# Kernel tuning notes

Hardware: AMD Instinct MI355X
Metric: run time of the kernel (lower is better)

The kernel has to match this reference:

```python
import jax, jax.numpy as jnp
import numpy as np

N = 20000      # nodes
E = 400000     # directed edges
F_IN = 256     # node features
H, C = 16, 32  # heads, per-head channels (out_channels + beta_on, beta_on=0)
OUT = 32       # out_channels
HID = 128      # 4 * out_channels


def setup_inputs() -> dict:
    key = jax.random.key(0)
    ks = jax.random.split(key, 14)
    s = 0.05
    return {
        "x": jax.random.normal(ks[0], (N, F_IN), jnp.float32),
        "edge_index": jax.random.randint(ks[1], (2, E), 0, N, jnp.int32),
        "W1": jax.random.normal(ks[2], (F_IN, H * C), jnp.float32) * s,
        "att_src1": jax.random.normal(ks[3], (H, C), jnp.float32) * s,
        "att_dst1": jax.random.normal(ks[4], (H, C), jnp.float32) * s,
        "b1": jax.random.normal(ks[5], (C,), jnp.float32) * s,
        "W2": jax.random.normal(ks[6], (F_IN, H * C), jnp.float32) * s,
        "att_src2": jax.random.normal(ks[7], (H, C), jnp.float32) * s,
        "att_dst2": jax.random.normal(ks[8], (H, C), jnp.float32) * s,
        "b2": jax.random.normal(ks[9], (C,), jnp.float32) * s,
        "lin1_w": jax.random.normal(ks[10], (F_IN, HID), jnp.float32) * s,
        "lin1_b": jax.random.normal(ks[11], (HID,), jnp.float32) * s,
        "lin2_w": jax.random.normal(ks[12], (HID, OUT), jnp.float32) * s,
        "lin2_b": jax.random.normal(ks[13], (OUT,), jnp.float32) * s,
    }


def gat_conv(x, W, att_src, att_dst, bias, src, dst):
    """PyG GATConv: heads=H, concat=False (mean over heads), no self loops.
    src = message source node per edge, dst = aggregation (central) node."""
    h = (x @ W).reshape(-1, H, C)                 # [N, H, C]
    a_s = jnp.sum(h * att_src, axis=-1)           # [N, H]
    a_d = jnp.sum(h * att_dst, axis=-1)           # [N, H]
    alpha = jax.nn.leaky_relu(a_s[src] + a_d[dst], 0.2)  # [E, H]
    # numerically-stable segment softmax over edges grouped by dst
    m = jax.lax.stop_gradient(jax.ops.segment_max(alpha, dst, num_segments=N))
    m = jnp.where(jnp.isfinite(m), m, 0.0)        # empty segments -> -inf
    ex = jnp.exp(alpha - m[dst])                  # [E, H]
    den = jax.ops.segment_sum(ex, dst, num_segments=N)   # [N, H]
    coef = ex / (den[dst] + 1e-16)                # [E, H]
    msg = h[src] * coef[:, :, None]               # [E, H, C]
    out = jax.ops.segment_sum(msg, dst, num_segments=N)  # [N, H, C]
    return out.mean(axis=1) + bias                # concat=False -> head mean


def reference(x, edge_index, W1, att_src1, att_dst1, b1, W2, att_src2, att_dst2,
              b2, lin1_w, lin1_b, lin2_w, lin2_b):
    src = edge_index[0]
    dst = edge_index[1]
    # conv1: flow='source_to_target' -> aggregate at edge_index[1]
    x_in = jax.nn.elu(gat_conv(x, W1, att_src1, att_dst1, b1, src, dst))
    # conv2: flow='target_to_source' -> aggregate at edge_index[0]
    x_out = jax.nn.elu(gat_conv(x, W2, att_src2, att_dst2, b2, dst, src))
    x1 = jax.nn.elu(x @ lin1_w + lin1_b)
    x_self = jax.nn.elu(x1 @ lin2_w + lin2_b)
    return (x_in, x_out, x_self)
```

## Files before the change

kernel.cpp:

```cpp
#include <hip/hip_runtime.h>
#include <math.h>

#define NN 20000
#define EE 400000
#define FIN 256
#define HH 16
#define CC 32
#define HC 512
#define H8W 1024
#define HIDN 128
#define OUTC 32
#define WT 1024
#define GEMM_B 1256

typedef unsigned short u16;
typedef unsigned char u8;
typedef __attribute__((ext_vector_type(8))) short short8v;
typedef __attribute__((ext_vector_type(4))) float f32x4;
typedef __attribute__((ext_vector_type(2))) float f32x2;

__device__ inline u16 f2bf(float f) {
  unsigned u = __builtin_bit_cast(unsigned, f);
  unsigned r = (u + 0x7fffu + ((u >> 16) & 1u)) >> 16;
  return (u16)r;
}

__device__ __forceinline__ void gload16(const u16* g, u16* l) {
  __builtin_amdgcn_global_load_lds(
      (const __attribute__((address_space(1))) unsigned int*)g,
      (__attribute__((address_space(3))) unsigned int*)l, 16, 0, 0);
}

__device__ __forceinline__ void fp8x8_fma2(uint2 hv, float w, f32x2* acc) {
  f32x2 w2; w2.x = w; w2.y = w;
  f32x2 p0 = __builtin_amdgcn_cvt_pk_f32_fp8(hv.x, false);
  f32x2 p1 = __builtin_amdgcn_cvt_pk_f32_fp8(hv.x, true);
  f32x2 p2 = __builtin_amdgcn_cvt_pk_f32_fp8(hv.y, false);
  f32x2 p3 = __builtin_amdgcn_cvt_pk_f32_fp8(hv.y, true);
  acc[0] += p0 * w2;
  acc[1] += p1 * w2;
  acc[2] += p2 * w2;
  acc[3] += p3 * w2;
}

__global__ void k_prep_hist(const float* __restrict__ x, u16* __restrict__ xb,
                            const float* __restrict__ W1, const float* __restrict__ W2,
                            u16* __restrict__ wtc,
                            const float* __restrict__ L1, u16* __restrict__ lt1,
                            const float* __restrict__ L2, u16* __restrict__ lt2,
                            const int* __restrict__ ei, int* __restrict__ cur) {
  int b = blockIdx.x, t = threadIdx.x;
  if (b < 2500) {
    int i = b * 256 + t;
    float4 v0 = ((const float4*)x)[i * 2];
    float4 v1 = ((const float4*)x)[i * 2 + 1];
    short8v o;
    o[0] = (short)f2bf(v0.x); o[1] = (short)f2bf(v0.y);
    o[2] = (short)f2bf(v0.z); o[3] = (short)f2bf(v0.w);
    o[4] = (short)f2bf(v1.x); o[5] = (short)f2bf(v1.y);
    o[6] = (short)f2bf(v1.z); o[7] = (short)f2bf(v1.w);
    *(short8v*)(xb + (size_t)i * 8) = o;
  } else if (b < 3524) {
    int i = (b - 2500) * 256 + t;
    int n = i >> 8, k = i & 255;
    wtc[i] = f2bf(n < 512 ? W1[k * HC + n] : W2[k * HC + (n - 512)]);
  } else if (b < 3652) {
    int i = (b - 3524) * 256 + t;
    int n = i >> 8, k = i & 255;
    lt1[i] = f2bf(L1[k * HIDN + n]);
  } else if (b < 3668) {
    int i = (b - 3652) * 256 + t;
    int n = i >> 7, k = i & 127;
    lt2[i] = f2bf(L2[k * OUTC + n]);
  } else {
    int e = (b - 3668) * 256 + t;
    if (e < EE) {
      atomicAdd(&cur[ei[EE + e]], 1);
      atomicAdd(&cur[NN + ei[e]], 1);
    }
  }
}

__device__ void scan_one(int* cur, int* off, int* part) {
  const int t = threadIdx.x;
  const int CHK = 20;
  int base = t * CHK;
  int loc[CHK];
  int s = 0;
#pragma unroll
  for (int i = 0; i < CHK; ++i) {
    int idx = base + i;
    int v = (idx < NN) ? cur[idx] : 0;
    loc[i] = s;
    s += v;
  }
  part[t] = s;
  __syncthreads();
  for (int d = 1; d < 1024; d <<= 1) {
    int v2 = (t >= d) ? part[t - d] : 0;
    __syncthreads();
    part[t] += v2;
    __syncthreads();
  }
  int cbase = part[t] - s;
#pragma unroll
  for (int i = 0; i < CHK; ++i) {
    int idx = base + i;
    if (idx < NN) {
      int o = cbase + loc[i];
      off[idx] = o;
      cur[idx] = o;
    }
  }
  if (t == 1023) off[NN] = part[1023];
}

__global__ __launch_bounds__(1024) void k_scan(int* cur, int* off1, int* off2) {
  __shared__ int part[1024];
  if (blockIdx.x == 0) scan_one(cur, off1, part);
  else                 scan_one(cur + NN, off2, part);
}

__global__ __launch_bounds__(256) void k_gemm_big(const u16* __restrict__ A,
                                                  const u16* __restrict__ Bt,
                                                  const float* __restrict__ as1,
                                                  const float* __restrict__ ad1,
                                                  const float* __restrict__ as2,
                                                  const float* __restrict__ ad2,
                                                  u8* __restrict__ h8,
                                                  float* __restrict__ a_sA,
                                                  float* __restrict__ a_dA,
                                                  const int* __restrict__ ei,
                                                  int* __restrict__ cur,
                                                  int* __restrict__ adj1,
                                                  int* __restrict__ adj2) {
  __shared__ u16 As[128 * 64];
  __shared__ u16 Bs[128 * 64];
  const int hw = blockIdx.x;
  const int logical = (hw & 7) * 157 + (hw >> 3);
  const int bm = (logical >> 3) * 128, bn = logical & 7;
  const int t = threadIdx.x;
  const int lane = t & 63, wave = t >> 6;
  const int wr = (wave >> 1) * 64, wc = (wave & 1) * 64;
  const int l15 = lane & 15, l4 = lane >> 4;
  const int rloc = lane >> 3;
  const int kc_src = (lane & 7) ^ rloc;
  const int K = FIN;

  for (int e = hw * 256 + t; e < EE; e += GEMM_B * 256) {
    int s1 = ei[e], d1 = ei[EE + e];
    int p1 = atomicAdd(&cur[d1], 1);
    adj1[p1] = s1;
    int p2 = atomicAdd(&cur[NN + s1], 1);
    adj2[p2] = d1;
  }

  f32x4 acc[4][4] = {};
  for (int k0 = 0; k0 < K; k0 += 64) {
    __syncthreads();
#pragma unroll
    for (int q = 0; q < 4; ++q) {
      const int rblk = q * 4 + wave;
      const int r = rblk * 8 + rloc;
      gload16(A + (size_t)(bm + r) * K + k0 + kc_src * 8, As + rblk * 512);
      gload16(Bt + (size_t)(bn * 128 + r) * K + k0 + kc_src * 8, Bs + rblk * 512);
    }
    __syncthreads();
#pragma unroll
    for (int kh = 0; kh < 2; ++kh) {
      const int kc = kh * 4 + l4;
      short8v af[4], bfr[4];
#pragma unroll
      for (int i = 0; i < 4; ++i) {
        int row = wr + i * 16 + l15;
        af[i] = *(const short8v*)(As + row * 64 + (kc ^ (row & 7)) * 8);
      }
#pragma unroll
      for (int j = 0; j < 4; ++j) {
        int row = wc + j * 16 + l15;
        bfr[j] = *(const short8v*)(Bs + row * 64 + (kc ^ (row & 7)) * 8);
      }
#pragma unroll
      for (int i = 0; i < 4; ++i)
#pragma unroll
        for (int j = 0; j < 4; ++j)
          acc[i][j] = __builtin_amdgcn_mfma_f32_16x16x32_bf16(af[i], bfr[j], acc[i][j], 0, 0, 0);
    }
  }

  const int conv = bn >> 2;
#pragma unroll
  for (int i = 0; i < 4; ++i)
#pragma unroll
    for (int j = 0; j < 4; ++j)
#pragma unroll
      for (int r = 0; r < 4; ++r) {
        int row = bm + wr + i * 16 + l4 * 4 + r;
        if (row >= NN) continue;
        int colb = bn * 128 + wc + j * 16 + l15;
        float v = acc[i][j][r];
        unsigned e8 = __builtin_amdgcn_cvt_pk_fp8_f32(v, v, 0, false);
        h8[(size_t)row * H8W + colb] = (u8)e8;
      }

  float asv[4], adv[4];
#pragma unroll
  for (int j = 0; j < 4; ++j) {
    int lc = (bn & 3) * 128 + wc + j * 16 + l15;
    int hh = lc >> 5, c = lc & 31;
    asv[j] = (conv ? as2 : as1)[hh * CC + c];
    adv[j] = (conv ? ad2 : ad1)[hh * CC + c];
  }
  const int hA = (bn & 3) * 4 + (wc >> 5);
  float* aS = a_sA + (size_t)conv * NN * HH;
  float* aD = a_dA + (size_t)conv * NN * HH;
#pragma unroll
  for (int i = 0; i < 4; ++i)
#pragma unroll
    for (int r = 0; r < 4; ++r) {
      float sAs = acc[i][0][r] * asv[0] + acc[i][1][r] * asv[1];
      float sAd = acc[i][0][r] * adv[0] + acc[i][1][r] * adv[1];
      float sBs = acc[i][2][r] * asv[2] + acc[i][3][r] * asv[3];
      float sBd = acc[i][2][r] * adv[2] + acc[i][3][r] * adv[3];
#pragma unroll
      for (int m = 1; m < 16; m <<= 1) {
        sAs += __shfl_xor(sAs, m);
        sAd += __shfl_xor(sAd, m);
        sBs += __shfl_xor(sBs, m);
        sBd += __shfl_xor(sBd, m);
      }
      int row = bm + wr + i * 16 + l4 * 4 + r;
      if (l15 == 0 && row < NN) {
        *(float2*)(aS + (size_t)row * HH + hA) = make_float2(sAs, sBs);
        *(float2*)(aD + (size_t)row * HH + hA) = make_float2(sAd, sBd);
      }
    }
}

__global__ __launch_bounds__(256) void k_self(const u16* __restrict__ A,
                                              const u16* __restrict__ lt1,
                                              const u16* __restrict__ lt2,
                                              const float* __restrict__ lin1_b,
                                              const float* __restrict__ lin2_b,
                                              float* __restrict__ outp) {
  __shared__ u16 smem[128 * 136];
  u16* As = smem;
  u16* Bs = smem + 128 * 64;
  const int t = threadIdx.x;
  const int lane = t & 63, wave = t >> 6;
  const int wr = (wave >> 1) * 64, wc = (wave & 1) * 64;
  const int bm = blockIdx.x * 128;
  const int l15 = lane & 15, l4 = lane >> 4;
  const int rloc = lane >> 3;
  const int kc_src = (lane & 7) ^ rloc;
  const int K = FIN;

  f32x4 acc[4][4] = {};
  for (int k0 = 0; k0 < K; k0 += 64) {
    __syncthreads();
#pragma unroll
    for (int q = 0; q < 4; ++q) {
      const int rblk = q * 4 + wave;
      const int r = rblk * 8 + rloc;
      gload16(A + (size_t)(bm + r) * K + k0 + kc_src * 8, As + rblk * 512);
      gload16(lt1 + (size_t)r * K + k0 + kc_src * 8, Bs + rblk * 512);
    }
    __syncthreads();
#pragma unroll
    for (int kh = 0; kh < 2; ++kh) {
      const int kc = kh * 4 + l4;
      short8v af[4], bfr[4];
#pragma unroll
      for (int i = 0; i < 4; ++i) {
        int row = wr + i * 16 + l15;
        af[i] = *(const short8v*)(As + row * 64 + (kc ^ (row & 7)) * 8);
      }
#pragma unroll
      for (int j = 0; j < 4; ++j) {
        int row = wc + j * 16 + l15;
        bfr[j] = *(const short8v*)(Bs + row * 64 + (kc ^ (row & 7)) * 8);
      }
#pragma unroll
      for (int i = 0; i < 4; ++i)
#pragma unroll
        for (int j = 0; j < 4; ++j)
          acc[i][j] = __builtin_amdgcn_mfma_f32_16x16x32_bf16(af[i], bfr[j], acc[i][j], 0, 0, 0);
    }
  }
  __syncthreads();
#pragma unroll
  for (int i = 0; i < 4; ++i)
#pragma unroll
    for (int j = 0; j < 4; ++j)
#pragma unroll
      for (int r = 0; r < 4; ++r) {
        int row = wr + i * 16 + l4 * 4 + r;
        int col = wc + j * 16 + l15;
        float v = acc[i][j][r] + lin1_b[col];
        v = v > 0.f ? v : (expf(v) - 1.f);
        smem[row * 136 + col] = f2bf(v);
      }
  __syncthreads();
  f32x4 acc2[2][2] = {};
#pragma unroll
  for (int kk = 0; kk < 4; ++kk) {
    short8v af[2], bfr[2];
#pragma unroll
    for (int i = 0; i < 2; ++i)
      af[i] = *(const short8v*)(smem + (wave * 32 + i * 16 + l15) * 136 + kk * 32 + l4 * 8);
#pragma unroll
    for (int j = 0; j < 2; ++j)
      bfr[j] = *(const short8v*)(lt2 + (size_t)(j * 16 + l15) * 128 + kk * 32 + l4 * 8);
#pragma unroll
    for (int i = 0; i < 2; ++i)
#pragma unroll
      for (int j = 0; j < 2; ++j)
        acc2[i][j] = __builtin_amdgcn_mfma_f32_16x16x32_bf16(af[i], bfr[j], acc2[i][j], 0, 0, 0);
  }
#pragma unroll
  for (int i = 0; i < 2; ++i)
#pragma unroll
    for (int j = 0; j < 2; ++j)
#pragma unroll
      for (int r = 0; r < 4; ++r) {
        int row = bm + wave * 32 + i * 16 + l4 * 4 + r;
        int col = j * 16 + l15;
        if (row < NN) {
          float v = acc2[i][j][r] + lin2_b[col];
          v = v > 0.f ? v : (expf(v) - 1.f);
          outp[(size_t)row * OUTC + col] = v;
        }
      }
}

__global__ __launch_bounds__(256) void k_edge(const int* __restrict__ adj1,
                                              const int* __restrict__ off1,
                                              const int* __restrict__ adj2,
                                              const int* __restrict__ off2,
                                              const float* __restrict__ a_sA,
                                              const float* __restrict__ a_dA,
                                              const u8* __restrict__ h8,
                                              const float* __restrict__ b1,
                                              const float* __restrict__ b2,
                                              float* __restrict__ out) {
  const int wv = threadIdx.x >> 6, lane = threadIdx.x & 63;
  const int gid = blockIdx.x * 4 + wv;
  const int conv = gid >= NN;
  const int node = gid - conv * NN;
  const int* __restrict__ adj = conv ? adj2 : adj1;
  const int* __restrict__ off = conv ? off2 : off1;
  const float* __restrict__ a_s = a_sA + (size_t)conv * NN * HH;
  const float* __restrict__ a_d = a_dA + (size_t)conv * NN * HH;
  const float* __restrict__ bias = conv ? b2 : b1;
  float* __restrict__ outp = out + (size_t)conv * NN * OUTC;
  const int e0 = off[node], e1 = off[node + 1];

  const int ea = lane >> 4, hh = lane & 15;
  const int h = lane >> 2, cg = lane & 3;
  const u8* hb = h8 + conv * HC + h * CC + cg * 8;
  const float adh = a_d[node * HH + hh];
  f32x2 acc0[4] = {}, acc1[4] = {};
  float den = 0.f;
  int p = e0;
  for (; p + 4 <= e1; p += 4) {
    int se = adj[p + ea];
    float al = a_s[se * HH + hh] + adh;
    al = al > 0.f ? al : 0.2f * al;
    float wgt = __expf(al);
    den += wgt;
    float w0 = __shfl(wgt, h);
    float w1 = __shfl(wgt, 16 + h);
    float w2 = __shfl(wgt, 32 + h);
    float w3 = __shfl(wgt, 48 + h);
    int s0 = adj[p], s1 = adj[p + 1], s2 = adj[p + 2], s3 = adj[p + 3];
    uint2 h0 = *(const uint2*)(hb + (size_t)s0 * H8W);
    uint2 h1 = *(const uint2*)(hb + (size_t)s1 * H8W);
    uint2 h2v = *(const uint2*)(hb + (size_t)s2 * H8W);
    uint2 h3 = *(const uint2*)(hb + (size_t)s3 * H8W);
    fp8x8_fma2(h0, w0, acc0);
    fp8x8_fma2(h1, w1, acc1);
    fp8x8_fma2(h2v, w2, acc0);
    fp8x8_fma2(h3, w3, acc1);
  }
  if (p < e1) {
    int pe = p + ea;
    float wgt = 0.f;
    if (pe < e1) {
      int se = adj[pe];
      float al = a_s[se * HH + hh] + adh;
      al = al > 0.f ? al : 0.2f * al;
      wgt = __expf(al);
    }
    den += wgt;
    float w0 = __shfl(wgt, h);
    float w1 = __shfl(wgt, 16 + h);
    float w2 = __shfl(wgt, 32 + h);
    {
      int s0 = adj[p];
      uint2 h0 = *(const uint2*)(hb + (size_t)s0 * H8W);
      fp8x8_fma2(h0, w0, acc0);
    }
    if (p + 1 < e1) {
      int s1 = adj[p + 1];
      uint2 h1 = *(const uint2*)(hb + (size_t)s1 * H8W);
      fp8x8_fma2(h1, w1, acc1);
    }
    if (p + 2 < e1) {
      int s2 = adj[p + 2];
      uint2 h2v = *(const uint2*)(hb + (size_t)s2 * H8W);
      fp8x8_fma2(h2v, w2, acc0);
    }
  }
  den += __shfl_xor(den, 16);
  den += __shfl_xor(den, 32);
  float inv = (1.f / 16.f) / (den + 1e-16f);
  const float ivh = __shfl(inv, h);
  float accf[8];
#pragma unroll
  for (int i = 0; i < 4; ++i) {
    f32x2 s2v = acc0[i] + acc1[i];
    accf[2 * i] = s2v.x * ivh;
    accf[2 * i + 1] = s2v.y * ivh;
  }
#pragma unroll
  for (int mk = 4; mk <= 32; mk <<= 1)
#pragma unroll
    for (int i = 0; i < 8; ++i) accf[i] += __shfl_xor(accf[i], mk);
  if (lane < 4) {
#pragma unroll
    for (int i = 0; i < 8; ++i) {
      int c = cg * 8 + i;
      float v = accf[i] + bias[c];
      v = v > 0.f ? v : (expf(v) - 1.f);
      outp[(size_t)node * OUTC + c] = v;
    }
  }
}

extern "C" void kernel_launch(void* const* d_in, const int* in_sizes, int n_in,
                              void* d_out, int out_size, void* d_ws, size_t ws_size,
                              hipStream_t stream) {
  const float* x = (const float*)d_in[0];
  const int* ei = (const int*)d_in[1];
  const float* W1 = (const float*)d_in[2];
  const float* att_src1 = (const float*)d_in[3];
  const float* att_dst1 = (const float*)d_in[4];
  const float* b1 = (const float*)d_in[5];
  const float* W2 = (const float*)d_in[6];
  const float* att_src2 = (const float*)d_in[7];
  const float* att_dst2 = (const float*)d_in[8];
  const float* b2 = (const float*)d_in[9];
  const float* lin1_w = (const float*)d_in[10];
  const float* lin1_b = (const float*)d_in[11];
  const float* lin2_w = (const float*)d_in[12];
  const float* lin2_b = (const float*)d_in[13];
  float* out = (float*)d_out;

  char* w = (char*)d_ws;
  u8* h8 = (u8*)w;          w += (size_t)NN * H8W;
  u16* x_bf = (u16*)w;      w += (size_t)NN * FIN * 2;
  u16* wtc = (u16*)w;       w += (size_t)WT * FIN * 2;
  u16* lt1 = (u16*)w;       w += (size_t)HIDN * FIN * 2;
  u16* lt2 = (u16*)w;       w += (size_t)OUTC * HIDN * 2;
  float* a_sA = (float*)w;  w += (size_t)2 * NN * HH * 4;
  float* a_dA = (float*)w;  w += (size_t)2 * NN * HH * 4;
  int* off1 = (int*)w;      w += (size_t)(NN + 1) * 4;
  int* off2 = (int*)w;      w += (size_t)(NN + 1) * 4;
  int* cur = (int*)w;       w += (size_t)2 * NN * 4;
  int* adj1 = (int*)w;      w += (size_t)EE * 4;
  int* adj2 = (int*)w;      w += (size_t)EE * 4;

  const int EB = (EE + 255) / 256;

  hipMemsetAsync(cur, 0, (size_t)2 * NN * 4, stream);
  k_prep_hist<<<3668 + EB, 256, 0, stream>>>(x, x_bf, W1, W2, wtc, lin1_w, lt1,
                                             lin2_w, lt2, ei, cur);
  k_scan<<<2, 1024, 0, stream>>>(cur, off1, off2);

  k_gemm_big<<<GEMM_B, 256, 0, stream>>>(x_bf, wtc, att_src1, att_dst1,
                                         att_src2, att_dst2, h8, a_sA, a_dA,
                                         ei, cur, adj1, adj2);
  k_self<<<157, 256, 0, stream>>>(x_bf, lt1, lt2, lin1_b, lin2_b,
                                  out + (size_t)2 * NN * OUTC);

  k_edge<<<2 * (NN / 4), 256, 0, stream>>>(adj1, off1, adj2, off2, a_sA, a_dA,
                                           h8, b1, b2, out);
}
```

Baseline: 217.7 us.

## Merge self-MLP kernel into big GEMM launch as extra blocks

The separate k_self launch is folded into k_gemm_big by adding 157 extra blocks that run the two-layer MLP, so one grid covers both GEMMs and the edge-bucketing loop is spread across all blocks. The intermediate LDS tile switches from a padded 136-stride layout to an XOR-swizzled 128-stride layout so shared memory stays at the GEMM's 32 KB. The goal is to remove one kernel launch and its tail, letting MLP blocks fill idle CUs at the end of the GEMM. The cost is a branchy kernel whose register use is the maximum of both paths, which could lower occupancy.

```diff
diff --git a/kernel.cpp b/kernel.cpp
--- a/kernel.cpp
+++ b/kernel.cpp
@@ -12,6 +12,7 @@
 #define OUTC 32
 #define WT 1024
 #define GEMM_B 1256
+#define TOT_B 1413
 
 typedef unsigned short u16;
 typedef unsigned char u8;
@@ -133,12 +134,16 @@
                                                   const int* __restrict__ ei,
                                                   int* __restrict__ cur,
                                                   int* __restrict__ adj1,
-                                                  int* __restrict__ adj2) {
-  __shared__ u16 As[128 * 64];
-  __shared__ u16 Bs[128 * 64];
+                                                  int* __restrict__ adj2,
+                                                  const u16* __restrict__ lt1,
+                                                  const u16* __restrict__ lt2,
+                                                  const float* __restrict__ lin1_b,
+                                                  const float* __restrict__ lin2_b,
+                                                  float* __restrict__ out3) {
+  __shared__ u16 smem[128 * 128];
+  u16* As = smem;
+  u16* Bs = smem + 128 * 64;
   const int hw = blockIdx.x;
-  const int logical = (hw & 7) * 157 + (hw >> 3);
-  const int bm = (logical >> 3) * 128, bn = logical & 7;
   const int t = threadIdx.x;
   const int lane = t & 63, wave = t >> 6;
   const int wr = (wave >> 1) * 64, wc = (wave & 1) * 64;
@@ -147,7 +152,7 @@
   const int kc_src = (lane & 7) ^ rloc;
   const int K = FIN;
 
-  for (int e = hw * 256 + t; e < EE; e += GEMM_B * 256) {
+  for (int e = hw * 256 + t; e < EE; e += TOT_B * 256) {
     int s1 = ei[e], d1 = ei[EE + e];
     int p1 = atomicAdd(&cur[d1], 1);
     adj1[p1] = s1;
@@ -155,182 +160,171 @@
     adj2[p2] = d1;
   }
 
-  f32x4 acc[4][4] = {};
-  for (int k0 = 0; k0 < K; k0 += 64) {
+  if (hw < GEMM_B) {
+    const int logical = (hw & 7) * 157 + (hw >> 3);
+    const int bm = (logical >> 3) * 128, bn = logical & 7;
+
+    f32x4 acc[4][4] = {};
+    for (int k0 = 0; k0 < K; k0 += 64) {
+      __syncthreads();
+#pragma unroll
+      for (int q = 0; q < 4; ++q) {
+        const int rblk = q * 4 + wave;
+        const int r = rblk * 8 + rloc;
+        gload16(A + (size_t)(bm + r) * K + k0 + kc_src * 8, As + rblk * 512);
+        gload16(Bt + (size_t)(bn * 128 + r) * K + k0 + kc_src * 8, Bs + rblk * 512);
+      }
+      __syncthreads();
+#pragma unroll
+      for (int kh = 0; kh < 2; ++kh) {
+        const int kc = kh * 4 + l4;
+        short8v af[4], bfr[4];
+#pragma unroll
+        for (int i = 0; i < 4; ++i) {
+          int row = wr + i * 16 + l15;
+          af[i] = *(const short8v*)(As + row * 64 + (kc ^ (row & 7)) * 8);
+        }
+#pragma unroll
+        for (int j = 0; j < 4; ++j) {
+          int row = wc + j * 16 + l15;
+          bfr[j] = *(const short8v*)(Bs + row * 64 + (kc ^ (row & 7)) * 8);
+        }
+#pragma unroll
+        for (int i = 0; i < 4; ++i)
+#pragma unroll
+          for (int j = 0; j < 4; ++j)
+            acc[i][j] = __builtin_amdgcn_mfma_f32_16x16x32_bf16(af[i], bfr[j], acc[i][j], 0, 0, 0);
+      }
+    }
+
+    const int conv = bn >> 2;
+#pragma unroll
+    for (int i = 0; i < 4; ++i)
+#pragma unroll
+      for (int j = 0; j < 4; ++j)
+#pragma unroll
+        for (int r = 0; r < 4; ++r) {
+          int row = bm + wr + i * 16 + l4 * 4 + r;
+          if (row >= NN) continue;
+          int colb = bn * 128 + wc + j * 16 + l15;
+          float v = acc[i][j][r];
+          unsigned e8 = __builtin_amdgcn_cvt_pk_fp8_f32(v, v, 0, false);
+          h8[(size_t)row * H8W + colb] = (u8)e8;
+        }
+
+    float asv[4], adv[4];
+#pragma unroll
+    for (int j = 0; j < 4; ++j) {
+      int lc = (bn & 3) * 128 + wc + j * 16 + l15;
+      int hh = lc >> 5, c = lc & 31;
+      asv[j] = (conv ? as2 : as1)[hh * CC + c];
+      adv[j] = (conv ? ad2 : ad1)[hh * CC + c];
+    }
+    const int hA = (bn & 3) * 4 + (wc >> 5);
+    float* aS = a_sA + (size_t)conv * NN * HH;
+    float* aD = a_dA + (size_t)conv * NN * HH;
+#pragma unroll
+    for (int i = 0; i < 4; ++i)
+#pragma unroll
+      for (int r = 0; r < 4; ++r) {
+        float sAs = acc[i][0][r] * asv[0] + acc[i][1][r] * asv[1];
+        float sAd = acc[i][0][r] * adv[0] + acc[i][1][r] * adv[1];
+        float sBs = acc[i][2][r] * asv[2] + acc[i][3][r] * asv[3];
+        float sBd = acc[i][2][r] * adv[2] + acc[i][3][r] * adv[3];
+#pragma unroll
+        for (int m = 1; m < 16; m <<= 1) {
+          sAs += __shfl_xor(sAs, m);
+          sAd += __shfl_xor(sAd, m);
+          sBs += __shfl_xor(sBs, m);
+          sBd += __shfl_xor(sBd, m);
+        }
+        int row = bm + wr + i * 16 + l4 * 4 + r;
+        if (l15 == 0 && row < NN) {
+          *(float2*)(aS + (size_t)row * HH + hA) = make_float2(sAs, sBs);
+          *(float2*)(aD + (size_t)row * HH + hA) = make_float2(sAd, sBd);
+        }
+      }
+  } else {
+    const int bm = (hw - GEMM_B) * 128;
+    f32x4 acc[4][4] = {};
+    for (int k0 = 0; k0 < K; k0 += 64) {
+      __syncthreads();
+#pragma unroll
+      for (int q = 0; q < 4; ++q) {
+        const int rblk = q * 4 + wave;
+        const int r = rblk * 8 + rloc;
+        gload16(A + (size_t)(bm + r) * K + k0 + kc_src * 8, As + rblk * 512);
+        gload16(lt1 + (size_t)r * K + k0 + kc_src * 8, Bs + rblk * 512);
+      }
+      __syncthreads();
+#pragma unroll
+      for (int kh = 0; kh < 2; ++kh) {
+        const int kc = kh * 4 + l4;
+        short8v af[4], bfr[4];
+#pragma unroll
+        for (int i = 0; i < 4; ++i) {
+          int row = wr + i * 16 + l15;
+          af[i] = *(const short8v*)(As + row * 64 + (kc ^ (row & 7)) * 8);
+        }
+#pragma unroll
+        for (int j = 0; j < 4; ++j) {
+          int row = wc + j * 16 + l15;
+          bfr[j] = *(const short8v*)(Bs + row * 64 + (kc ^ (row & 7)) * 8);
+        }
+#pragma unroll
+        for (int i = 0; i < 4; ++i)
+#pragma unroll
+          for (int j = 0; j < 4; ++j)
+            acc[i][j] = __builtin_amdgcn_mfma_f32_16x16x32_bf16(af[i], bfr[j], acc[i][j], 0, 0, 0);
+      }
+    }
     __syncthreads();
 #pragma unroll
-    for (int q = 0; q < 4; ++q) {
-      const int rblk = q * 4 + wave;
-      const int r = rblk * 8 + rloc;
-      gload16(A + (size_t)(bm + r) * K + k0 + kc_src * 8, As + rblk * 512);
-      gload16(Bt + (size_t)(bn * 128 + r) * K + k0 + kc_src * 8, Bs + rblk * 512);
-    }
+    for (int i = 0; i < 4; ++i)
+#pragma unroll
+      for (int j = 0; j < 4; ++j)
+#pragma unroll
+        for (int r = 0; r < 4; ++r) {
+          int row = wr + i * 16 + l4 * 4 + r;
+          int col = wc + j * 16 + l15;
+          float v = acc[i][j][r] + lin1_b[col];
+          v = v > 0.f ? v : (expf(v) - 1.f);
+          smem[row * 128 + ((((col >> 3) ^ (row & 7))) << 3) + (col & 7)] = f2bf(v);
+        }
     __syncthreads();
-#pragma unroll
-    for (int kh = 0; kh < 2; ++kh) {
-      const int kc = kh * 4 + l4;
-      short8v af[4], bfr[4];
-#pragma unroll
-      for (int i = 0; i < 4; ++i) {
-        int row = wr + i * 16 + l15;
-        af[i] = *(const short8v*)(As + row * 64 + (kc ^ (row & 7)) * 8);
-      }
-#pragma unroll
-      for (int j = 0; j < 4; ++j) {
-        int row = wc + j * 16 + l15;
-        bfr[j] = *(const short8v*)(Bs + row * 64 + (kc ^ (row & 7)) * 8);
-      }
-#pragma unroll
-      for (int i = 0; i < 4; ++i)
-#pragma unroll
-        for (int j = 0; j < 4; ++j)
-          acc[i][j] = __builtin_amdgcn_mfma_f32_16x16x32_bf16(af[i], bfr[j], acc[i][j], 0, 0, 0);
-    }
-  }
-
-  const int conv = bn >> 2;
-#pragma unroll
-  for (int i = 0; i < 4; ++i)
-#pragma unroll
-    for (int j = 0; j < 4; ++j)
-#pragma unroll
-      for (int r = 0; r < 4; ++r) {
-        int row = bm + wr + i * 16 + l4 * 4 + r;
-        if (row >= NN) continue;
-        int colb = bn * 128 + wc + j * 16 + l15;
-        float v = acc[i][j][r];
-        unsigned e8 = __builtin_amdgcn_cvt_pk_fp8_f32(v, v, 0, false);
-        h8[(size_t)row * H8W + colb] = (u8)e8;
-      }
-
-  float asv[4], adv[4];
-#pragma unroll
-  for (int j = 0; j < 4; ++j) {
-    int lc = (bn & 3) * 128 + wc + j * 16 + l15;
-    int hh = lc >> 5, c = lc & 31;
-    asv[j] = (conv ? as2 : as1)[hh * CC + c];
-    adv[j] = (conv ? ad2 : ad1)[hh * CC + c];
-  }
-  const int hA = (bn & 3) * 4 + (wc >> 5);
-  float* aS = a_sA + (size_t)conv * NN * HH;
-  float* aD = a_dA + (size_t)conv * NN * HH;
-#pragma unroll
-  for (int i = 0; i < 4; ++i)
-#pragma unroll
-    for (int r = 0; r < 4; ++r) {
-      float sAs = acc[i][0][r] * asv[0] + acc[i][1][r] * asv[1];
-      float sAd = acc[i][0][r] * adv[0] + acc[i][1][r] * adv[1];
-      float sBs = acc[i][2][r] * asv[2] + acc[i][3][r] * asv[3];
-      float sBd = acc[i][2][r] * adv[2] + acc[i][3][r] * adv[3];
-#pragma unroll
-      for (int m = 1; m < 16; m <<= 1) {
-        sAs += __shfl_xor(sAs, m);
-        sAd += __shfl_xor(sAd, m);
-        sBs += __shfl_xor(sBs, m);
-        sBd += __shfl_xor(sBd, m);
-      }
-      int row = bm + wr + i * 16 + l4 * 4 + r;
-      if (l15 == 0 && row < NN) {
-        *(float2*)(aS + (size_t)row * HH + hA) = make_float2(sAs, sBs);
-        *(float2*)(aD + (size_t)row * HH + hA) = make_float2(sAd, sBd);
-      }
-    }
-}
-
-__global__ __launch_bounds__(256) void k_self(const u16* __restrict__ A,
-                                              const u16* __restrict__ lt1,
-                                              const u16* __restrict__ lt2,
-                                              const float* __restrict__ lin1_b,
-                                              const float* __restrict__ lin2_b,
-                                              float* __restrict__ outp) {
-  __shared__ u16 smem[128 * 136];
-  u16* As = smem;
-  u16* Bs = smem + 128 * 64;
-  const int t = threadIdx.x;
-  const int lane = t & 63, wave = t >> 6;
-  const int wr = (wave >> 1) * 64, wc = (wave & 1) * 64;
-  const int bm = blockIdx.x * 128;
-  const int l15 = lane & 15, l4 = lane >> 4;
-  const int rloc = lane >> 3;
-  const int kc_src = (lane & 7) ^ rloc;
-  const int K = FIN;
-
-  f32x4 acc[4][4] = {};
-  for (int k0 = 0; k0 < K; k0 += 64) {
-    __syncthreads();
-#pragma unroll
-    for (int q = 0; q < 4; ++q) {
-      const int rblk = q * 4 + wave;
-      const int r = rblk * 8 + rloc;
-      gload16(A + (size_t)(bm + r) * K + k0 + kc_src * 8, As + rblk * 512);
-      gload16(lt1 + (size_t)r * K + k0 + kc_src * 8, Bs + rblk * 512);
-    }
-    __syncthreads();
-#pragma unroll
-    for (int kh = 0; kh < 2; ++kh) {
-      const int kc = kh * 4 + l4;
-      short8v af[4], bfr[4];
-#pragma unroll
-      for (int i = 0; i < 4; ++i) {
-        int row = wr + i * 16 + l15;
-        af[i] = *(const short8v*)(As + row * 64 + (kc ^ (row & 7)) * 8);
-      }
-#pragma unroll
-      for (int j = 0; j < 4; ++j) {
-        int row = wc + j * 16 + l15;
-        bfr[j] = *(const short8v*)(Bs + row * 64 + (kc ^ (row & 7)) * 8);
-      }
-#pragma unroll
-      for (int i = 0; i < 4; ++i)
-#pragma unroll
-        for (int j = 0; j < 4; ++j)
-          acc[i][j] = __builtin_amdgcn_mfma_f32_16x16x32_bf16(af[i], bfr[j], acc[i][j], 0, 0, 0);
-    }
-  }
-  __syncthreads();
-#pragma unroll
-  for (int i = 0; i < 4; ++i)
-#pragma unroll
-    for (int j = 0; j < 4; ++j)
-#pragma unroll
-      for (int r = 0; r < 4; ++r) {
-        int row = wr + i * 16 + l4 * 4 + r;
-        int col = wc + j * 16 + l15;
-        float v = acc[i][j][r] + lin1_b[col];
-        v = v > 0.f ? v : (expf(v) - 1.f);
-        smem[row * 136 + col] = f2bf(v);
-      }
-  __syncthreads();
-  f32x4 acc2[2][2] = {};
-#pragma unroll
-  for (int kk = 0; kk < 4; ++kk) {
-    short8v af[2], bfr[2];
+    f32x4 acc2[2][2] = {};
+#pragma unroll
+    for (int kk = 0; kk < 4; ++kk) {
+      short8v af[2], bfr[2];
+#pragma unroll
+      for (int i = 0; i < 2; ++i) {
+        int row2 = wave * 32 + i * 16 + l15;
+        af[i] = *(const short8v*)(smem + row2 * 128 + (((kk * 4 + l4) ^ (row2 & 7)) << 3));
+      }
+#pragma unroll
+      for (int j = 0; j < 2; ++j)
+        bfr[j] = *(const short8v*)(lt2 + (size_t)(j * 16 + l15) * 128 + kk * 32 + l4 * 8);
+#pragma unroll
+      for (int i = 0; i < 2; ++i)
+#pragma unroll
+        for (int j = 0; j < 2; ++j)
+          acc2[i][j] = __builtin_amdgcn_mfma_f32_16x16x32_bf16(af[i], bfr[j], acc2[i][j], 0, 0, 0);
+    }
 #pragma unroll
     for (int i = 0; i < 2; ++i)
-      af[i] = *(const short8v*)(smem + (wave * 32 + i * 16 + l15) * 136 + kk * 32 + l4 * 8);
-#pragma unroll
-    for (int j = 0; j < 2; ++j)
-      bfr[j] = *(const short8v*)(lt2 + (size_t)(j * 16 + l15) * 128 + kk * 32 + l4 * 8);
-#pragma unroll
-    for (int i = 0; i < 2; ++i)
 #pragma unroll
       for (int j = 0; j < 2; ++j)
-        acc2[i][j] = __builtin_amdgcn_mfma_f32_16x16x32_bf16(af[i], bfr[j], acc2[i][j], 0, 0, 0);
-  }
-#pragma unroll
-  for (int i = 0; i < 2; ++i)
-#pragma unroll
-    for (int j = 0; j < 2; ++j)
-#pragma unroll
-      for (int r = 0; r < 4; ++r) {
-        int row = bm + wave * 32 + i * 16 + l4 * 4 + r;
-        int col = j * 16 + l15;
-        if (row < NN) {
-          float v = acc2[i][j][r] + lin2_b[col];
-          v = v > 0.f ? v : (expf(v) - 1.f);
-          outp[(size_t)row * OUTC + col] = v;
-        }
-      }
+#pragma unroll
+        for (int r = 0; r < 4; ++r) {
+          int row = bm + wave * 32 + i * 16 + l4 * 4 + r;
+          int col = j * 16 + l15;
+          if (row < NN) {
+            float v = acc2[i][j][r] + lin2_b[col];
+            v = v > 0.f ? v : (expf(v) - 1.f);
+            out3[(size_t)row * OUTC + col] = v;
+          }
+        }
+  }
 }
 
 __global__ __launch_bounds__(256) void k_edge(const int* __restrict__ adj1,
@@ -477,11 +471,11 @@
                                              lin2_w, lt2, ei, cur);
   k_scan<<<2, 1024, 0, stream>>>(cur, off1, off2);
 
-  k_gemm_big<<<GEMM_B, 256, 0, stream>>>(x_bf, wtc, att_src1, att_dst1,
-                                         att_src2, att_dst2, h8, a_sA, a_dA,
-                                         ei, cur, adj1, adj2);
-  k_self<<<157, 256, 0, stream>>>(x_bf, lt1, lt2, lin1_b, lin2_b,
-                                  out + (size_t)2 * NN * OUTC);
+  k_gemm_big<<<TOT_B, 256, 0, stream>>>(x_bf, wtc, att_src1, att_dst1,
+                                        att_src2, att_dst2, h8, a_sA, a_dA,
+                                        ei, cur, adj1, adj2, lt1, lt2,
+                                        lin1_b, lin2_b,
+                                        out + (size_t)2 * NN * OUTC);
 
   k_edge<<<2 * (NN / 4), 256, 0, stream>>>(adj1, off1, adj2, off2, a_sA, a_dA,
                                            h8, b1, b2, out);
```

Result: faster. 208.6 us (median of 2 runs) (-4.2%).
